# Kernel tuning notes

Hardware: AMD Instinct MI355X
Metric: run time of the kernel (lower is better)

Reference implementation:

```python
import jax, jax.numpy as jnp
import numpy as np

B, T, E = 2, 2048, 2048
H, KV, D = 16, 4, 128
N_REP = H // KV
WINDOW = 512
BASE_THETA = 10000.0
MIN_VAL = -1e9


def _rope_cos_sin(seq_len, dim, dtype):
    inv_freq = 1.0 / (BASE_THETA ** (jnp.arange(0, dim, 2, dtype=jnp.float32) / dim))
    ang = jnp.arange(seq_len, dtype=jnp.float32)[:, None] * inv_freq[None, :]  # [T, D/2]
    return jnp.cos(ang).astype(dtype), jnp.sin(ang).astype(dtype)


def _apply_rope(x, cos, sin):
    # x: [B, T, h, D]; rotate-half convention
    x1, x2 = jnp.split(x, 2, axis=-1)
    c = cos[None, :, None, :]
    s = sin[None, :, None, :]
    return jnp.concatenate([x1 * c - x2 * s, x2 * c + x1 * s], axis=-1)


def setup_inputs() -> dict:
    key = jax.random.key(0)
    k1, k2, k3, k4, k5 = jax.random.split(key, 5)
    std = 0.02 / np.sqrt(2 * 24)
    return {
        "x": jax.random.normal(k1, (B, T, E), dtype=jnp.float32),
        "Wq": jax.random.normal(k2, (H * D, E), dtype=jnp.float32) * std,
        "Wk": jax.random.normal(k3, (KV * D, E), dtype=jnp.float32) * std,
        "Wv": jax.random.normal(k4, (KV * D, E), dtype=jnp.float32) * std,
        "Wo": jax.random.normal(k5, (E, E), dtype=jnp.float32) * std,
    }


def reference(x, Wq, Wk, Wv, Wo):
    b, t, e = x.shape
    scale = 1.0 / jnp.sqrt(jnp.float32(D))

    q = (x @ Wq.T).reshape(b, t, H, D)
    k = (x @ Wk.T).reshape(b, t, KV, D)
    v = (x @ Wv.T).reshape(b, t, KV, D)

    cos, sin = _rope_cos_sin(t, D, x.dtype)
    q = _apply_rope(q, cos, sin)
    k = _apply_rope(k, cos, sin)

    # GQA: repeat kv heads to match query heads
    k = jnp.repeat(k, N_REP, axis=2)  # [B, T, H, D]
    v = jnp.repeat(v, N_REP, axis=2)

    scores = jnp.einsum("bqhd,bkhd->bhqk", q, k) * scale  # [B, H, T, T]

    # sliding-window causal additive mask (offset=0)
    rows = jnp.arange(t)[:, None]
    cols = jnp.arange(t)[None, :]
    valid = (cols <= rows) & ((rows - cols) < WINDOW)
    mask = jnp.where(valid, 0.0, MIN_VAL).astype(x.dtype)  # [T, T]
    scores = scores + mask[None, None, :, :]

    attn = jax.nn.softmax(scores, axis=-1)
    out = jnp.einsum("bhqk,bkhd->bqhd", attn, v).reshape(b, t, H * D)
    return out @ Wo.T
```

## Files before the change

### kernel.cpp

```cpp
#include <hip/hip_runtime.h>
#include <hip/hip_bf16.h>
#include <cstdint>

#define TSEQ 2048
#define NB   2
#define NH   16
#define NKV  4
#define HD   128
#define EMB  2048
#define WIN  512

typedef unsigned short u16;
typedef __attribute__((ext_vector_type(8))) short s16x8;
typedef __attribute__((ext_vector_type(4))) float f32x4;
typedef __attribute__((ext_vector_type(4))) unsigned short u16x4;
typedef __attribute__((ext_vector_type(8))) unsigned short u16x8;

__device__ __forceinline__ u16 f2bf(float x) {
    unsigned u = __builtin_bit_cast(unsigned, x);
    u += 0x7fffu + ((u >> 16) & 1u);
    return (u16)(u >> 16);
}
__device__ __forceinline__ float bf2f(u16 u) {
    return __builtin_bit_cast(float, ((unsigned)u) << 16);
}
__device__ __forceinline__ float ex2(float x) {
    return __builtin_amdgcn_exp2f(x);
}

__device__ __forceinline__ void gld_lds16(const void* g, void* l) {
    __builtin_amdgcn_global_load_lds(
        (__attribute__((address_space(1))) void*)(void*)(g),
        (__attribute__((address_space(3))) void*)(l),
        16, 0, 0);
}

__device__ __forceinline__ f32x4 mfma16(s16x8 a, s16x8 b, f32x4 c) {
    return __builtin_amdgcn_mfma_f32_16x16x32_bf16(a, b, c, 0, 0, 0);
}

template <int CTRL>
__device__ __forceinline__ float dpp_movf(float x) {
    return __builtin_bit_cast(float,
        __builtin_amdgcn_update_dpp(0, __builtin_bit_cast(int, x), CTRL, 0xF, 0xF, true));
}
__device__ __forceinline__ float dpp_max16(float x) {
    x = fmaxf(x, dpp_movf<0xB1>(x));
    x = fmaxf(x, dpp_movf<0x4E>(x));
    x = fmaxf(x, dpp_movf<0x128>(x));
    x = fmaxf(x, dpp_movf<0x124>(x));
    return x;
}
__device__ __forceinline__ float dpp_sum16(float x) {
    x += dpp_movf<0xB1>(x);
    x += dpp_movf<0x4E>(x);
    x += dpp_movf<0x128>(x);
    x += dpp_movf<0x124>(x);
    return x;
}

__global__ void cast_all(const float* __restrict__ x,  const float* __restrict__ wq,
                         const float* __restrict__ wk, const float* __restrict__ wv,
                         const float* __restrict__ wo,
                         u16* __restrict__ xb, u16* __restrict__ wqb,
                         u16* __restrict__ wkvb, u16* __restrict__ wob,
                         float* __restrict__ tab) {
    if (blockIdx.x >= 18432) {
        int i = (blockIdx.x - 18432) * 256 + threadIdx.x;
        int t = i >> 6, d = i & 63;
        float inv = __expf(-(float)d * (9.210340371976184f / 64.0f));
        float s, c;
        sincosf((float)t * inv, &s, &c);
        tab[i] = c;
        tab[131072 + i] = s;
        return;
    }
    long i = ((long)blockIdx.x * 256 + threadIdx.x) * 4;
    const float* s; u16* d; long off;
    if (i < 8388608L)        { s = x;  d = xb;             off = i; }
    else if (i < 12582912L)  { s = wq; d = wqb;            off = i - 8388608L; }
    else if (i < 13631488L)  { s = wk; d = wkvb;           off = i - 12582912L; }
    else if (i < 14680064L)  { s = wv; d = wkvb + 1048576; off = i - 13631488L; }
    else                     { s = wo; d = wob;            off = i - 14680064L; }
    float4 v = *(const float4*)(s + off);
    u16x4 o;
    o[0] = f2bf(v.x); o[1] = f2bf(v.y); o[2] = f2bf(v.z); o[3] = f2bf(v.w);
    *(u16x4*)(d + off) = o;
}

template <int MODE>
__global__ __launch_bounds__(256) void gemm_bt(const u16* __restrict__ A, const u16* __restrict__ B,
                                               void* __restrict__ Cp, u16* __restrict__ vtp,
                                               u16* __restrict__ kp,
                                               int M, int N, int K) {
    __shared__ __align__(16) char smem[MODE == 3 ? 17408 : 16384];
    u16* As = (u16*)smem;
    u16* Bs = As + 4096;
    const int tid  = threadIdx.x;
    const int lane = tid & 63;
    const int w    = tid >> 6;
    const int l15  = lane & 15;
    const int quad = lane >> 4;
    const int wr   = w >> 1, wc = w & 1;

    const int srow  = w * 32 + (lane >> 2);
    const int cbyte = (lane & 3) * 16;
    const char* ag0 = (const char*)(A + (size_t)(blockIdx.y * 128 + srow) * K) + cbyte;
    const char* ag1 = ag0 + (size_t)16 * K * 2;
    const char* bg0 = (const char*)(B + (size_t)(blockIdx.x * 128 + srow) * K) + cbyte;
    const char* bg1 = bg0 + (size_t)16 * K * 2;
    char* al0 = (char*)As + (w * 32) * 64;
    char* al1 = al0 + 16 * 64;
    char* bl0 = (char*)Bs + (w * 32) * 64;
    char* bl1 = bl0 + 16 * 64;

    f32x4 acc[4][4];
#pragma unroll
    for (int i = 0; i < 4; i++)
#pragma unroll
        for (int j = 0; j < 4; j++)
            acc[i][j] = f32x4{0.f, 0.f, 0.f, 0.f};

    for (int k0 = 0; k0 < K; k0 += 32) {
        gld_lds16(ag0, al0);
        gld_lds16(ag1, al1);
        gld_lds16(bg0, bl0);
        gld_lds16(bg1, bl1);
        ag0 += 64; ag1 += 64; bg0 += 64; bg1 += 64;
        __syncthreads();
        s16x8 af[4], bf[4];
#pragma unroll
        for (int i = 0; i < 4; i++)
            af[i] = *(const s16x8*)(As + (wr * 64 + i * 16 + l15) * 32 + quad * 8);
#pragma unroll
        for (int j = 0; j < 4; j++)
            bf[j] = *(const s16x8*)(Bs + (wc * 64 + j * 16 + l15) * 32 + quad * 8);
#pragma unroll
        for (int i = 0; i < 4; i++)
#pragma unroll
            for (int j = 0; j < 4; j++)
                acc[i][j] = mfma16(af[i], bf[j], acc[i][j]);
        __syncthreads();
    }

    const int row0 = blockIdx.y * 128 + wr * 64;
    const int col0 = blockIdx.x * 128 + wc * 64 + l15;

    if (MODE == 0) {
#pragma unroll
        for (int i = 0; i < 4; i++)
#pragma unroll
            for (int j = 0; j < 4; j++)
#pragma unroll
                for (int r = 0; r < 4; r++)
                    ((float*)Cp)[(size_t)(row0 + i * 16 + quad * 4 + r) * N + col0 + j * 16] =
                        acc[i][j][r];
    } else {
        if (blockIdx.x < 16) {
#pragma unroll
            for (int i = 0; i < 4; i++)
#pragma unroll
                for (int j = 0; j < 4; j++)
#pragma unroll
                    for (int r = 0; r < 4; r++)
                        ((u16*)Cp)[(size_t)(row0 + i * 16 + quad * 4 + r) * 2048 + col0 + j * 16] =
                            f2bf(acc[i][j][r]);
        } else if (blockIdx.x < 20) {
            const int kcol0 = col0 - 2048;
#pragma unroll
            for (int i = 0; i < 4; i++)
#pragma unroll
                for (int j = 0; j < 4; j++)
#pragma unroll
                    for (int r = 0; r < 4; r++)
                        kp[(size_t)(row0 + i * 16 + quad * 4 + r) * 512 + kcol0 + j * 16] =
                            f2bf(acc[i][j][r]);
        } else {
            const int kvi  = blockIdx.x - 20;
            const int bb   = (blockIdx.y * 128) >> 11;
            const int tl0  = (blockIdx.y * 128) & (TSEQ - 1);
            u16* tr = (u16*)smem;
#pragma unroll
            for (int p = 0; p < 2; p++) {
                __syncthreads();
                if (wc == p) {
#pragma unroll
                    for (int i = 0; i < 4; i++)
#pragma unroll
                        for (int j = 0; j < 4; j++)
#pragma unroll
                            for (int r = 0; r < 4; r++)
                                tr[(j * 16 + l15) * 136 + wr * 64 + i * 16 + quad * 4 + r] =
                                    f2bf(acc[i][j][r]);
                }
                __syncthreads();
#pragma unroll
                for (int s = 0; s < 4; s++) {
                    int slot = s * 256 + tid;
                    int dr = slot >> 4;
                    int tc = slot & 15;
                    u16x8 val = *(const u16x8*)(tr + dr * 136 + tc * 8);
                    *(u16x8*)(vtp + ((size_t)((bb * NKV + kvi) * HD + p * 64 + dr)) * TSEQ +
                              tl0 + tc * 8) = val;
                }
            }
        }
    }
}

__global__ void rope_k(u16* __restrict__ buf, const float* __restrict__ tab) {
    int i = blockIdx.x * 256 + threadIdx.x;
    int d   = i & 63;
    int hh  = (i >> 6) & 3;
    int row = i >> 8;
    int t   = row & (TSEQ - 1);
    size_t base = (size_t)row * 512 + hh * HD + d;
    float x1 = bf2f(buf[base]);
    float x2 = bf2f(buf[base + 64]);
    float c = tab[t * 64 + d];
    float s = tab[131072 + t * 64 + d];
    buf[base]      = f2bf(x1 * c - x2 * s);
    buf[base + 64] = f2bf(x2 * c + x1 * s);
}

__global__ __launch_bounds__(256, 3) void attn_kernel(const u16* __restrict__ qb, const u16* __restrict__ kb,
                                                      const u16* __restrict__ vt, const float* __restrict__ tab,
                                                      u16* __restrict__ ao) {
    __shared__ __align__(16) char smem[40960];
    u16* ks = (u16*)smem;
    u16* vs = (u16*)(smem + 16384);
    u16* Pl = (u16*)(smem + 32768);

    const int tid  = threadIdx.x;
    const int w    = tid >> 6;
    const int lane = tid & 63;
    const int l15  = lane & 15;
    const int quad = lane >> 4;
    const int id   = blockIdx.x;
    const int kv   = id & 3;
    const int b    = (id >> 2) & 1;
    const int q0   = (id >> 3) * 16;
    const int h    = kv * 4 + w;
    u16* Pw = Pl + w * 1024;
    const float scale2 = 0.1275174089593282f;

    const u16* kbase = kb + (size_t)b * TSEQ * 512 + kv * HD;
    const u16* vbase = vt + (size_t)(b * NKV + kv) * HD * TSEQ;

    s16x8 aq[4];
    {
        const u16* qrow = qb + (size_t)(b * TSEQ + q0 + l15) * EMB + h * HD + quad * 8;
        const float* ct = tab + (size_t)(q0 + l15) * 64 + quad * 8;
        float qf[4][8], cs[2][8], sn[2][8];
        *(float4*)(&cs[0][0]) = *(const float4*)(ct);
        *(float4*)(&cs[0][4]) = *(const float4*)(ct + 4);
        *(float4*)(&cs[1][0]) = *(const float4*)(ct + 32);
        *(float4*)(&cs[1][4]) = *(const float4*)(ct + 36);
        *(float4*)(&sn[0][0]) = *(const float4*)(ct + 131072);
        *(float4*)(&sn[0][4]) = *(const float4*)(ct + 131076);
        *(float4*)(&sn[1][0]) = *(const float4*)(ct + 131104);
        *(float4*)(&sn[1][4]) = *(const float4*)(ct + 131108);
#pragma unroll
        for (int c = 0; c < 4; c++)
#pragma unroll
            for (int e = 0; e < 8; e++)
                qf[c][e] = bf2f(qrow[c * 32 + e]);
#pragma unroll
        for (int c = 0; c < 2; c++)
#pragma unroll
            for (int e = 0; e < 8; e++) {
                float x1 = qf[c][e], x2 = qf[c + 2][e];
                qf[c][e]     = x1 * cs[c][e] - x2 * sn[c][e];
                qf[c + 2][e] = x2 * cs[c][e] + x1 * sn[c][e];
            }
#pragma unroll
        for (int c = 0; c < 4; c++)
#pragma unroll
            for (int e = 0; e < 8; e++)
                aq[c][e] = (short)f2bf(qf[c][e]);
    }

    f32x4 o[8];
#pragma unroll
    for (int n = 0; n < 8; n++) o[n] = f32x4{0.f, 0.f, 0.f, 0.f};
    float mrow[4] = {-1e30f, -1e30f, -1e30f, -1e30f};
    float lrow[4] = {0.f, 0.f, 0.f, 0.f};

    int kb0 = q0 - (WIN - 1);
    if (kb0 < 0) kb0 = 0;
    kb0 &= ~63;

    for (int kbi = kb0; kbi <= q0 + 15; kbi += 64) {
#pragma unroll
        for (int s = 0; s < 4; s++) {
            int slot = s * 256 + tid;
            int i    = slot >> 4;
            int lc   = (slot & 15) ^ (i & 7);
            gld_lds16(kbase + (size_t)(kbi + i) * 512 + lc * 8, (char*)ks + slot * 16);
        }
#pragma unroll
        for (int s = 0; s < 4; s++) {
            int slot = s * 256 + tid;
            int d    = slot >> 3;
            int lc   = (slot & 7) ^ (d & 7);
            gld_lds16(vbase + (size_t)d * TSEQ + kbi + lc * 8, (char*)vs + slot * 16);
        }
        __syncthreads();

        f32x4 sv[4];
#pragma unroll
        for (int kt = 0; kt < 4; kt++) sv[kt] = f32x4{0.f, 0.f, 0.f, 0.f};
#pragma unroll
        for (int c = 0; c < 4; c++) {
            s16x8 bk[4];
#pragma unroll
            for (int kt = 0; kt < 4; kt++) {
                int sc = (c * 4 + quad) ^ (l15 & 7);
                bk[kt] = *(const s16x8*)(ks + (kt * 16 + l15) * 128 + sc * 8);
            }
#pragma unroll
            for (int kt = 0; kt < 4; kt++)
                sv[kt] = mfma16(aq[c], bk[kt], sv[kt]);
        }

        const bool full = (kbi >= q0 - 496) && (kbi + 63 <= q0);
        float alpha[4], p[4][4];
#pragma unroll
        for (int r = 0; r < 4; r++) {
            const int row = q0 + quad * 4 + r;
            float v[4];
            if (full) {
#pragma unroll
                for (int kt = 0; kt < 4; kt++) v[kt] = sv[kt][r] * scale2;
            } else {
#pragma unroll
                for (int kt = 0; kt < 4; kt++) {
                    int cidx = kbi + kt * 16 + l15;
                    v[kt] = (cidx <= row && row - cidx < WIN) ? sv[kt][r] * scale2 : -1e30f;
                }
            }
            float mx = fmaxf(fmaxf(v[0], v[1]), fmaxf(v[2], v[3]));
            mx = dpp_max16(mx);
            float mnew = fmaxf(mrow[r], mx);
            alpha[r] = ex2(mrow[r] - mnew);
            float e0 = ex2(v[0] - mnew);
            float e1 = ex2(v[1] - mnew);
            float e2 = ex2(v[2] - mnew);
            float e3 = ex2(v[3] - mnew);
            float rs = (e0 + e1) + (e2 + e3);
            rs = dpp_sum16(rs);
            lrow[r] = lrow[r] * alpha[r] + rs;
            mrow[r] = mnew;
            p[0][r] = e0; p[1][r] = e1; p[2][r] = e2; p[3][r] = e3;
        }
#pragma unroll
        for (int n = 0; n < 8; n++) {
            o[n][0] *= alpha[0]; o[n][1] *= alpha[1];
            o[n][2] *= alpha[2]; o[n][3] *= alpha[3];
        }

#pragma unroll
        for (int r = 0; r < 4; r++)
#pragma unroll
            for (int kt = 0; kt < 4; kt++)
                Pw[(kt >> 1) * 512 + (quad * 4 + r) * 32 + (kt & 1) * 16 + l15] = f2bf(p[kt][r]);
        asm volatile("s_waitcnt lgkmcnt(0)" ::: "memory");
        s16x8 ap0 = *(const s16x8*)(Pw + l15 * 32 + quad * 8);
        s16x8 ap1 = *(const s16x8*)(Pw + 512 + l15 * 32 + quad * 8);

#pragma unroll
        for (int n = 0; n < 8; n++) {
            int sc = quad ^ (l15 & 7);
            s16x8 bv = *(const s16x8*)(vs + (n * 16 + l15) * 64 + sc * 8);
            o[n] = mfma16(ap0, bv, o[n]);
        }
#pragma unroll
        for (int n = 0; n < 8; n++) {
            int sc = (4 + quad) ^ (l15 & 7);
            s16x8 bv = *(const s16x8*)(vs + (n * 16 + l15) * 64 + sc * 8);
            o[n] = mfma16(ap1, bv, o[n]);
        }
        __syncthreads();
    }

    float linv[4];
#pragma unroll
    for (int r = 0; r < 4; r++) linv[r] = 1.0f / lrow[r];
    u16* Ow = (u16*)(smem + w * 4352);
#pragma unroll
    for (int n = 0; n < 8; n++)
#pragma unroll
        for (int r = 0; r < 4; r++)
            Ow[(quad * 4 + r) * 136 + n * 16 + l15] = f2bf(o[n][r] * linv[r]);
    asm volatile("s_waitcnt lgkmcnt(0)" ::: "memory");
#pragma unroll
    for (int s = 0; s < 4; s++) {
        int row = s * 4 + quad;
        u16x8 val = *(const u16x8*)(Ow + row * 136 + l15 * 8);
        *(u16x8*)(ao + (size_t)(b * TSEQ + q0 + row) * EMB + h * HD + l15 * 8) = val;
    }
}

extern "C" void kernel_launch(void* const* d_in, const int* in_sizes, int n_in,
                              void* d_out, int out_size, void* d_ws, size_t ws_size,
                              hipStream_t stream) {
    const float* x  = (const float*)d_in[0];
    const float* Wq = (const float*)d_in[1];
    const float* Wk = (const float*)d_in[2];
    const float* Wv = (const float*)d_in[3];
    const float* Wo = (const float*)d_in[4];
    float* out = (float*)d_out;

    u16* ws   = (u16*)d_ws;
    u16* xb   = ws;
    u16* wqb  = ws + 8388608L;
    u16* wkvb = ws + 12582912L;
    u16* wob  = ws + 14680064L;
    u16* qb   = ws + 18874368L;
    u16* kbuf = ws + 27262976L;
    u16* vt   = ws + 29360128L;
    float* tab = (float*)(ws + 31457280L);
    u16* ao   = xb;

    cast_all<<<18944, 256, 0, stream>>>(x, Wq, Wk, Wv, Wo, xb, wqb, wkvb, wob, tab);

    gemm_bt<3><<<dim3(24, 32), 256, 0, stream>>>(xb, wqb, qb, vt, kbuf, 4096, 3072, 2048);

    rope_k<<<4096, 256, 0, stream>>>(kbuf, tab);

    attn_kernel<<<1024, 256, 0, stream>>>(qb, kbuf, vt, tab, ao);

    gemm_bt<0><<<dim3(16, 32), 256, 0, stream>>>(ao, wob, out, nullptr, nullptr, 4096, 2048, 2048);
}
```

Measured before the change: 287.6 us.

## Switch GEMM to 32x32x16 MFMA with K=64 tiles and XOR-swizzled LDS

Rewrites the bf16 GEMM inner loop to use 32x32x16 MFMA instructions instead of 16x16x32, doubles the K step per LDS stage to 64, and XOR-swizzles the LDS row layout to avoid bank conflicts on fragment reads. The aim is fewer barriers per K, higher MFMA efficiency and conflict-free LDS reads. Epilogues are remapped to the 32x32 accumulator layout. LDS use doubles to 32KB, which could lower occupancy.

```diff
diff --git a/kernel.cpp b/kernel.cpp
--- a/kernel.cpp
+++ b/kernel.cpp
@@ -13,6 +13,7 @@
 typedef unsigned short u16;
 typedef __attribute__((ext_vector_type(8))) short s16x8;
 typedef __attribute__((ext_vector_type(4))) float f32x4;
+typedef __attribute__((ext_vector_type(16))) float f32x16;
 typedef __attribute__((ext_vector_type(4))) unsigned short u16x4;
 typedef __attribute__((ext_vector_type(8))) unsigned short u16x8;
 
@@ -37,6 +38,9 @@
 
 __device__ __forceinline__ f32x4 mfma16(s16x8 a, s16x8 b, f32x4 c) {
     return __builtin_amdgcn_mfma_f32_16x16x32_bf16(a, b, c, 0, 0, 0);
+}
+__device__ __forceinline__ f32x16 mfma32(s16x8 a, s16x8 b, f32x16 c) {
+    return __builtin_amdgcn_mfma_f32_32x32x16_bf16(a, b, c, 0, 0, 0);
 }
 
 template <int CTRL>
@@ -93,105 +97,134 @@
                                                void* __restrict__ Cp, u16* __restrict__ vtp,
                                                u16* __restrict__ kp,
                                                int M, int N, int K) {
-    __shared__ __align__(16) char smem[MODE == 3 ? 17408 : 16384];
-    u16* As = (u16*)smem;
-    u16* Bs = As + 4096;
+    __shared__ __align__(16) u16 smem[16384];
+    u16* As = smem;
+    u16* Bs = smem + 8192;
     const int tid  = threadIdx.x;
     const int lane = tid & 63;
     const int w    = tid >> 6;
-    const int l15  = lane & 15;
-    const int quad = lane >> 4;
+    const int l31  = lane & 31;
+    const int half = lane >> 5;
     const int wr   = w >> 1, wc = w & 1;
 
-    const int srow  = w * 32 + (lane >> 2);
-    const int cbyte = (lane & 3) * 16;
-    const char* ag0 = (const char*)(A + (size_t)(blockIdx.y * 128 + srow) * K) + cbyte;
-    const char* ag1 = ag0 + (size_t)16 * K * 2;
-    const char* bg0 = (const char*)(B + (size_t)(blockIdx.x * 128 + srow) * K) + cbyte;
-    const char* bg1 = bg0 + (size_t)16 * K * 2;
-    char* al0 = (char*)As + (w * 32) * 64;
-    char* al1 = al0 + 16 * 64;
-    char* bl0 = (char*)Bs + (w * 32) * 64;
-    char* bl1 = bl0 + 16 * 64;
-
-    f32x4 acc[4][4];
-#pragma unroll
-    for (int i = 0; i < 4; i++)
-#pragma unroll
-        for (int j = 0; j < 4; j++)
-            acc[i][j] = f32x4{0.f, 0.f, 0.f, 0.f};
-
-    for (int k0 = 0; k0 < K; k0 += 32) {
-        gld_lds16(ag0, al0);
-        gld_lds16(ag1, al1);
-        gld_lds16(bg0, bl0);
-        gld_lds16(bg1, bl1);
-        ag0 += 64; ag1 += 64; bg0 += 64; bg1 += 64;
+    const int srow   = w * 8 + (lane >> 3);
+    const int schunk = lane & 7;
+    const u16* agp[4];
+    const u16* bgp[4];
+#pragma unroll
+    for (int s = 0; s < 4; s++) {
+        const int row = s * 32 + srow;
+        const int sig = ((row >> 1) ^ (row >> 2)) & 7;
+        agp[s] = A + (size_t)(blockIdx.y * 128 + row) * K + (schunk ^ sig) * 8;
+        bgp[s] = B + (size_t)(blockIdx.x * 128 + row) * K + (schunk ^ sig) * 8;
+    }
+
+    int sigA[2], sigB[2];
+#pragma unroll
+    for (int i = 0; i < 2; i++) {
+        const int ra = wr * 64 + i * 32 + l31;
+        sigA[i] = ((ra >> 1) ^ (ra >> 2)) & 7;
+        const int rb = wc * 64 + i * 32 + l31;
+        sigB[i] = ((rb >> 1) ^ (rb >> 2)) & 7;
+    }
+
+    f32x16 acc[2][2];
+#pragma unroll
+    for (int i = 0; i < 2; i++)
+#pragma unroll
+        for (int j = 0; j < 2; j++)
+#pragma unroll
+            for (int r = 0; r < 16; r++)
+                acc[i][j][r] = 0.f;
+
+    for (int k0 = 0; k0 < K; k0 += 64) {
+#pragma unroll
+        for (int s = 0; s < 4; s++) {
+            gld_lds16(agp[s], (char*)As + (s * 32 + w * 8) * 128);
+            agp[s] += 64;
+        }
+#pragma unroll
+        for (int s = 0; s < 4; s++) {
+            gld_lds16(bgp[s], (char*)Bs + (s * 32 + w * 8) * 128);
+            bgp[s] += 64;
+        }
         __syncthreads();
-        s16x8 af[4], bf[4];
-#pragma unroll
-        for (int i = 0; i < 4; i++)
-            af[i] = *(const s16x8*)(As + (wr * 64 + i * 16 + l15) * 32 + quad * 8);
-#pragma unroll
-        for (int j = 0; j < 4; j++)
-            bf[j] = *(const s16x8*)(Bs + (wc * 64 + j * 16 + l15) * 32 + quad * 8);
-#pragma unroll
-        for (int i = 0; i < 4; i++)
-#pragma unroll
-            for (int j = 0; j < 4; j++)
-                acc[i][j] = mfma16(af[i], bf[j], acc[i][j]);
+        s16x8 af[2][4], bf[2][4];
+#pragma unroll
+        for (int i = 0; i < 2; i++)
+#pragma unroll
+            for (int ks = 0; ks < 4; ks++)
+                af[i][ks] = *(const s16x8*)((char*)As + (wr * 64 + i * 32 + l31) * 128 +
+                                            ((half + ks * 2) ^ sigA[i]) * 16);
+#pragma unroll
+        for (int j = 0; j < 2; j++)
+#pragma unroll
+            for (int ks = 0; ks < 4; ks++)
+                bf[j][ks] = *(const s16x8*)((char*)Bs + (wc * 64 + j * 32 + l31) * 128 +
+                                            ((half + ks * 2) ^ sigB[j]) * 16);
+#pragma unroll
+        for (int ks = 0; ks < 4; ks++)
+#pragma unroll
+            for (int i = 0; i < 2; i++)
+#pragma unroll
+                for (int j = 0; j < 2; j++)
+                    acc[i][j] = mfma32(af[i][ks], bf[j][ks], acc[i][j]);
         __syncthreads();
     }
 
     const int row0 = blockIdx.y * 128 + wr * 64;
-    const int col0 = blockIdx.x * 128 + wc * 64 + l15;
+    const int col0 = blockIdx.x * 128 + wc * 64 + l31;
 
     if (MODE == 0) {
 #pragma unroll
-        for (int i = 0; i < 4; i++)
-#pragma unroll
-            for (int j = 0; j < 4; j++)
-#pragma unroll
-                for (int r = 0; r < 4; r++)
-                    ((float*)Cp)[(size_t)(row0 + i * 16 + quad * 4 + r) * N + col0 + j * 16] =
-                        acc[i][j][r];
+        for (int i = 0; i < 2; i++)
+#pragma unroll
+            for (int j = 0; j < 2; j++)
+#pragma unroll
+                for (int r = 0; r < 16; r++) {
+                    const int crow = row0 + i * 32 + (r & 3) + 8 * (r >> 2) + 4 * half;
+                    ((float*)Cp)[(size_t)crow * N + col0 + j * 32] = acc[i][j][r];
+                }
     } else {
         if (blockIdx.x < 16) {
 #pragma unroll
-            for (int i = 0; i < 4; i++)
-#pragma unroll
-                for (int j = 0; j < 4; j++)
-#pragma unroll
-                    for (int r = 0; r < 4; r++)
-                        ((u16*)Cp)[(size_t)(row0 + i * 16 + quad * 4 + r) * 2048 + col0 + j * 16] =
-                            f2bf(acc[i][j][r]);
+            for (int i = 0; i < 2; i++)
+#pragma unroll
+                for (int j = 0; j < 2; j++)
+#pragma unroll
+                    for (int r = 0; r < 16; r++) {
+                        const int crow = row0 + i * 32 + (r & 3) + 8 * (r >> 2) + 4 * half;
+                        ((u16*)Cp)[(size_t)crow * 2048 + col0 + j * 32] = f2bf(acc[i][j][r]);
+                    }
         } else if (blockIdx.x < 20) {
             const int kcol0 = col0 - 2048;
 #pragma unroll
-            for (int i = 0; i < 4; i++)
-#pragma unroll
-                for (int j = 0; j < 4; j++)
-#pragma unroll
-                    for (int r = 0; r < 4; r++)
-                        kp[(size_t)(row0 + i * 16 + quad * 4 + r) * 512 + kcol0 + j * 16] =
-                            f2bf(acc[i][j][r]);
+            for (int i = 0; i < 2; i++)
+#pragma unroll
+                for (int j = 0; j < 2; j++)
+#pragma unroll
+                    for (int r = 0; r < 16; r++) {
+                        const int crow = row0 + i * 32 + (r & 3) + 8 * (r >> 2) + 4 * half;
+                        kp[(size_t)crow * 512 + kcol0 + j * 32] = f2bf(acc[i][j][r]);
+                    }
         } else {
-            const int kvi  = blockIdx.x - 20;
-            const int bb   = (blockIdx.y * 128) >> 11;
-            const int tl0  = (blockIdx.y * 128) & (TSEQ - 1);
-            u16* tr = (u16*)smem;
+            const int kvi = blockIdx.x - 20;
+            const int bb  = (blockIdx.y * 128) >> 11;
+            const int tl0 = (blockIdx.y * 128) & (TSEQ - 1);
+            u16* tr = smem;
 #pragma unroll
             for (int p = 0; p < 2; p++) {
                 __syncthreads();
                 if (wc == p) {
 #pragma unroll
-                    for (int i = 0; i < 4; i++)
-#pragma unroll
-                        for (int j = 0; j < 4; j++)
-#pragma unroll
-                            for (int r = 0; r < 4; r++)
-                                tr[(j * 16 + l15) * 136 + wr * 64 + i * 16 + quad * 4 + r] =
-                                    f2bf(acc[i][j][r]);
+                    for (int i = 0; i < 2; i++)
+#pragma unroll
+                        for (int j = 0; j < 2; j++)
+#pragma unroll
+                            for (int r = 0; r < 16; r++) {
+                                const int tl = wr * 64 + i * 32 + (r & 3) + 8 * (r >> 2) + 4 * half;
+                                tr[(j * 32 + l31) * 136 + tl] = f2bf(acc[i][j][r]);
+                            }
                 }
                 __syncthreads();
 #pragma unroll
```

Measured after the change: 267.8 us. 6.9% less time.
